# Optimization experiments

Measured on AMD Instinct MI355X. Metric: run time of the kernel, lower is better.

## Reference

```python
import jax, jax.numpy as jnp
import numpy as np

N_NODES = 50000
N_EDGES = 640000
D_IN, D_HID, D_OUT = 128, 256, 2


def setup_inputs() -> dict:
    key = jax.random.key(0)
    ks = jax.random.split(key, 8)
    node_features = jax.random.normal(ks[0], (N_NODES, D_IN), dtype=jnp.float32)
    src = jax.random.randint(ks[1], (N_EDGES,), 0, N_NODES)
    dst = jax.random.randint(ks[2], (N_EDGES,), 0, N_NODES)
    s_in = 1.0 / np.sqrt(D_IN)
    s_hid = 1.0 / np.sqrt(D_HID)
    return {
        "node_features": node_features,
        "src": src,
        "dst": dst,
        "W1_self": jax.random.normal(ks[3], (D_IN, D_HID), dtype=jnp.float32) * s_in,
        "W1_neigh": jax.random.normal(ks[4], (D_IN, D_HID), dtype=jnp.float32) * s_in,
        "b1": jnp.zeros((D_HID,), dtype=jnp.float32),
        "W2_self": jax.random.normal(ks[5], (D_HID, D_OUT), dtype=jnp.float32) * s_hid,
        "W2_neigh": jax.random.normal(ks[6], (D_HID, D_OUT), dtype=jnp.float32) * s_hid,
        "b2": jnp.zeros((D_OUT,), dtype=jnp.float32),
    }


def _sage_mean(x, src, dst, W_self, W_neigh, b, n_nodes):
    # gather source-node features along edges, mean-reduce into destinations
    msg = x[src]                                                  # [E, D]
    agg = jax.ops.segment_sum(msg, dst, num_segments=n_nodes)     # [N, D]
    deg = jax.ops.segment_sum(jnp.ones((src.shape[0], 1), x.dtype), dst,
                              num_segments=n_nodes)               # [N, 1]
    h_neigh = agg / jnp.maximum(deg, 1.0)
    return x @ W_self + h_neigh @ W_neigh + b


def reference(node_features, src, dst, W1_self, W1_neigh, b1, W2_self, W2_neigh, b2):
    h = _sage_mean(node_features, src, dst, W1_self, W1_neigh, b1, N_NODES)
    h = jax.nn.relu(h)
    logits = _sage_mean(h, src, dst, W2_self, W2_neigh, b2, N_NODES)
    return logits
```

## Files before the change

kernel.cpp:

```cpp
#include <hip/hip_runtime.h>

#define D_IN 128
#define D_HID 256
#define CH 1024
#define MPAD 50048

typedef short bf16x8 __attribute__((ext_vector_type(8)));
typedef float f32x4 __attribute__((ext_vector_type(4)));

__device__ __forceinline__ unsigned short f2bf_rne(float x) {
  unsigned int u = __float_as_uint(x);
  unsigned int r = (u + 0x7FFFu + ((u >> 16) & 1u)) >> 16;
  return (unsigned short)r;
}
__device__ __forceinline__ float bf2f(unsigned short b) {
  return __uint_as_float(((unsigned int)b) << 16);
}

__global__ void k_hist(const int* __restrict__ dst, int* __restrict__ deg, int E) {
  int e = blockIdx.x * blockDim.x + threadIdx.x;
  if (e < E) atomicAdd(&deg[dst[e]], 1);
}

__global__ __launch_bounds__(256) void k_csum(const int* __restrict__ deg,
                                              int* __restrict__ csum, int n) {
  __shared__ int ws[4];
  int t = threadIdx.x, lane = t & 63, w = t >> 6;
  int base = blockIdx.x * CH + t * 4;
  int s = 0;
  #pragma unroll
  for (int j = 0; j < 4; ++j) { int i = base + j; s += (i < n) ? deg[i] : 0; }
  #pragma unroll
  for (int off = 32; off > 0; off >>= 1) s += __shfl_down(s, off, 64);
  if (lane == 0) ws[w] = s;
  __syncthreads();
  if (t == 0) csum[blockIdx.x] = ws[0] + ws[1] + ws[2] + ws[3];
}

__global__ void k_coff(const int* __restrict__ csum, int* __restrict__ coff, int nb) {
  int lane = threadIdx.x & 63;
  int v = (lane < nb) ? csum[lane] : 0;
  int x = v;
  #pragma unroll
  for (int off = 1; off < 64; off <<= 1) {
    int u = __shfl_up(x, off, 64);
    if (lane >= off) x += u;
  }
  if (lane < nb) coff[lane] = x - v;
}

__global__ __launch_bounds__(256) void k_scanw(const int* __restrict__ deg,
                                               const int* __restrict__ coff,
                                               int* __restrict__ rs, int n) {
  __shared__ int ws[4];
  int t = threadIdx.x, lane = t & 63, w = t >> 6;
  int base = blockIdx.x * CH + t * 4;
  int d[4];
  #pragma unroll
  for (int j = 0; j < 4; ++j) { int i = base + j; d[j] = (i < n) ? deg[i] : 0; }
  int tt = d[0] + d[1] + d[2] + d[3];
  int x = tt;
  #pragma unroll
  for (int off = 1; off < 64; off <<= 1) {
    int u = __shfl_up(x, off, 64);
    if (lane >= off) x += u;
  }
  if (lane == 63) ws[w] = x;
  __syncthreads();
  if (t == 0) { int s = 0;
    #pragma unroll
    for (int j = 0; j < 4; ++j) { int tmp = ws[j]; ws[j] = s; s += tmp; } }
  __syncthreads();
  int excl = ws[w] + (x - tt) + coff[blockIdx.x];
  #pragma unroll
  for (int j = 0; j < 4; ++j) {
    int i = base + j;
    excl += d[j];
    if (i < n) rs[i + 1] = excl;
  }
  if (blockIdx.x == 0 && t == 0) rs[0] = 0;
}

__global__ void k_scatter(const int* __restrict__ src, const int* __restrict__ dst,
                          const int* __restrict__ rs, int* __restrict__ cursor,
                          int* __restrict__ esrc, int E) {
  int e = blockIdx.x * blockDim.x + threadIdx.x;
  if (e < E) {
    int d = dst[e];
    int pos = rs[d] + atomicAdd(&cursor[d], 1);
    esrc[pos] = src[e];
  }
}

__global__ __launch_bounds__(256) void k_convW(const float* __restrict__ W1s,
                                               const float* __restrict__ W1n,
                                               unsigned short* __restrict__ Bth,
                                               unsigned short* __restrict__ Btl) {
  int k = blockIdx.x;
  int col = threadIdx.x;
  float w = (k < 128) ? W1s[(size_t)k * D_HID + col]
                      : W1n[(size_t)(k - 128) * D_HID + col];
  unsigned short hi = f2bf_rne(w);
  unsigned short lo = f2bf_rne(w - bf2f(hi));
  Bth[(size_t)col * 256 + k] = hi;
  Btl[(size_t)col * 256 + k] = lo;
}

__global__ __launch_bounds__(256) void k_convX(const float* __restrict__ X,
                                               unsigned short* __restrict__ Ah,
                                               unsigned short* __restrict__ Al,
                                               int n) {
  int row = blockIdx.x * 4 + (threadIdx.x >> 6);
  int lane = threadIdx.x & 63;
  unsigned short* ah = Ah + (size_t)row * 256 + lane * 2;
  unsigned short* al = Al + (size_t)row * 256 + lane * 2;
  if (row < n) {
    float2 v = *(const float2*)(X + (size_t)row * D_IN + lane * 2);
    unsigned short hx = f2bf_rne(v.x), hy = f2bf_rne(v.y);
    unsigned short lx = f2bf_rne(v.x - bf2f(hx)), ly = f2bf_rne(v.y - bf2f(hy));
    *(ushort2*)ah = make_ushort2(hx, hy);
    *(ushort2*)al = make_ushort2(lx, ly);
  } else {
    ushort2 z = make_ushort2(0, 0);
    *(ushort2*)ah = z; *(ushort2*)(ah + 128) = z;
    *(ushort2*)al = z; *(ushort2*)(al + 128) = z;
  }
}

__global__ void k_agg1(const float* __restrict__ X, const int* __restrict__ rs,
                       const int* __restrict__ esrc,
                       unsigned short* __restrict__ Ah,
                       unsigned short* __restrict__ Al, int n) {
  int wid = (blockIdx.x * blockDim.x + threadIdx.x) >> 6;
  int lane = threadIdx.x & 63;
  if (wid >= n) return;
  int s0 = rs[wid], s1 = rs[wid + 1];
  float ax0 = 0.f, ay0 = 0.f, ax1 = 0.f, ay1 = 0.f;
  int e = s0;
  for (; e + 3 < s1; e += 4) {
    int i0 = esrc[e + 0], i1 = esrc[e + 1], i2 = esrc[e + 2], i3 = esrc[e + 3];
    float2 v0 = *(const float2*)(X + (size_t)i0 * D_IN + lane * 2);
    float2 v1 = *(const float2*)(X + (size_t)i1 * D_IN + lane * 2);
    float2 v2 = *(const float2*)(X + (size_t)i2 * D_IN + lane * 2);
    float2 v3 = *(const float2*)(X + (size_t)i3 * D_IN + lane * 2);
    ax0 += v0.x; ay0 += v0.y;
    ax1 += v1.x; ay1 += v1.y;
    ax0 += v2.x; ay0 += v2.y;
    ax1 += v3.x; ay1 += v3.y;
  }
  for (; e < s1; ++e) {
    int s = esrc[e];
    float2 v = *(const float2*)(X + (size_t)s * D_IN + lane * 2);
    ax0 += v.x; ay0 += v.y;
  }
  int d = s1 - s0;
  float inv = 1.0f / (float)(d > 1 ? d : 1);
  float mx = (ax0 + ax1) * inv, my = (ay0 + ay1) * inv;
  unsigned short hx = f2bf_rne(mx), hy = f2bf_rne(my);
  unsigned short lx = f2bf_rne(mx - bf2f(hx)), ly = f2bf_rne(my - bf2f(hy));
  *(ushort2*)(Ah + (size_t)wid * 256 + 128 + lane * 2) = make_ushort2(hx, hy);
  *(ushort2*)(Al + (size_t)wid * 256 + 128 + lane * 2) = make_ushort2(lx, ly);
}

#define AS1 __attribute__((address_space(1)))
#define AS3 __attribute__((address_space(3)))

__global__ __launch_bounds__(256, 3) void k_gemm1(
    const unsigned short* __restrict__ Ah, const unsigned short* __restrict__ Al,
    const unsigned short* __restrict__ Bth, const unsigned short* __restrict__ Btl,
    const float* __restrict__ b1, const float* __restrict__ W2s,
    const float* __restrict__ W2n, float* __restrict__ SP) {
  __shared__ unsigned short sAh[128][32];
  __shared__ unsigned short sAl[128][32];
  __shared__ unsigned short sBh[128][32];
  __shared__ unsigned short sBl[128][32];

  const int tid = threadIdx.x;
  const int w = tid >> 6;
  const int l = tid & 63;
  const int wm = w & 1, wn = w >> 1;
  const int m0 = blockIdx.x * 128;
  const int n0 = blockIdx.y * 128;

  f32x4 acc[4][4];
  #pragma unroll
  for (int i = 0; i < 4; ++i)
    #pragma unroll
    for (int j = 0; j < 4; ++j) acc[i][j] = (f32x4)0.f;

  const int rsub = l >> 2;
  const int ksub = (l & 3) * 8;
  const int g = l >> 4;
  const int c = l & 15;
  const int kb = g * 8;

  for (int kt = 0; kt < 256; kt += 32) {
    #pragma unroll
    for (int j = 0; j < 2; ++j) {
      int r = w * 32 + j * 16;
      const unsigned short* ga = Ah + (size_t)(m0 + r + rsub) * 256 + kt + ksub;
      const unsigned short* gb = Al + (size_t)(m0 + r + rsub) * 256 + kt + ksub;
      const unsigned short* gc = Bth + (size_t)(n0 + r + rsub) * 256 + kt + ksub;
      const unsigned short* gd = Btl + (size_t)(n0 + r + rsub) * 256 + kt + ksub;
      __builtin_amdgcn_global_load_lds((AS1 const void*)ga, (AS3 void*)&sAh[r][0], 16, 0, 0);
      __builtin_amdgcn_global_load_lds((AS1 const void*)gb, (AS3 void*)&sAl[r][0], 16, 0, 0);
      __builtin_amdgcn_global_load_lds((AS1 const void*)gc, (AS3 void*)&sBh[r][0], 16, 0, 0);
      __builtin_amdgcn_global_load_lds((AS1 const void*)gd, (AS3 void*)&sBl[r][0], 16, 0, 0);
    }
    __syncthreads();

    bf16x8 ahi[4], alo[4];
    #pragma unroll
    for (int mi = 0; mi < 4; ++mi) {
      int arow = wm * 64 + mi * 16 + c;
      ahi[mi] = *(const bf16x8*)(&sAh[arow][kb]);
      alo[mi] = *(const bf16x8*)(&sAl[arow][kb]);
    }
    #pragma unroll
    for (int ni = 0; ni < 4; ++ni) {
      int bcol = wn * 64 + ni * 16 + c;
      bf16x8 bhi = *(const bf16x8*)(&sBh[bcol][kb]);
      bf16x8 blo = *(const bf16x8*)(&sBl[bcol][kb]);
      #pragma unroll
      for (int mi = 0; mi < 4; ++mi) {
        acc[mi][ni] = __builtin_amdgcn_mfma_f32_16x16x32_bf16(ahi[mi], bhi, acc[mi][ni], 0, 0, 0);
        acc[mi][ni] = __builtin_amdgcn_mfma_f32_16x16x32_bf16(ahi[mi], blo, acc[mi][ni], 0, 0, 0);
        acc[mi][ni] = __builtin_amdgcn_mfma_f32_16x16x32_bf16(alo[mi], bhi, acc[mi][ni], 0, 0, 0);
      }
    }
    __syncthreads();
  }

  float b1v[4]; float2 w2sv[4], w2nv[4];
  #pragma unroll
  for (int ni = 0; ni < 4; ++ni) {
    int col = n0 + wn * 64 + ni * 16 + c;
    b1v[ni] = b1[col];
    w2sv[ni] = *(const float2*)(W2s + (size_t)col * 2);
    w2nv[ni] = *(const float2*)(W2n + (size_t)col * 2);
  }
  #pragma unroll
  for (int mi = 0; mi < 4; ++mi) {
    #pragma unroll
    for (int j = 0; j < 4; ++j) {
      float s0 = 0.f, s1 = 0.f, p0 = 0.f, p1 = 0.f;
      #pragma unroll
      for (int ni = 0; ni < 4; ++ni) {
        float h = fmaxf(acc[mi][ni][j] + b1v[ni], 0.f);
        s0 += h * w2sv[ni].x; s1 += h * w2sv[ni].y;
        p0 += h * w2nv[ni].x; p1 += h * w2nv[ni].y;
      }
      #pragma unroll
      for (int off = 1; off < 16; off <<= 1) {
        s0 += __shfl_xor(s0, off, 64);
        s1 += __shfl_xor(s1, off, 64);
        p0 += __shfl_xor(p0, off, 64);
        p1 += __shfl_xor(p1, off, 64);
      }
      if (c == 0) {
        int row = m0 + wm * 64 + mi * 16 + g * 4 + j;
        float* sp = SP + (size_t)row * 4;
        atomicAdd(sp + 0, s0);
        atomicAdd(sp + 1, s1);
        atomicAdd(sp + 2, p0);
        atomicAdd(sp + 3, p1);
      }
    }
  }
}

__global__ void k_agg2(const float* __restrict__ SP,
                       const int* __restrict__ rs, const int* __restrict__ esrc,
                       const float* __restrict__ b2,
                       float* __restrict__ out, int n) {
  int nid = blockIdx.x * blockDim.x + threadIdx.x;
  if (nid >= n) return;
  int s0 = rs[nid], s1 = rs[nid + 1];
  float a00 = 0.f, a01 = 0.f, a10 = 0.f, a11 = 0.f;
  int e = s0;
  for (; e + 3 < s1; e += 4) {
    int i0 = esrc[e + 0], i1 = esrc[e + 1], i2 = esrc[e + 2], i3 = esrc[e + 3];
    float2 p0 = *(const float2*)(SP + (size_t)i0 * 4 + 2);
    float2 p1 = *(const float2*)(SP + (size_t)i1 * 4 + 2);
    float2 p2 = *(const float2*)(SP + (size_t)i2 * 4 + 2);
    float2 p3 = *(const float2*)(SP + (size_t)i3 * 4 + 2);
    a00 += p0.x; a01 += p0.y;
    a10 += p1.x; a11 += p1.y;
    a00 += p2.x; a01 += p2.y;
    a10 += p3.x; a11 += p3.y;
  }
  for (; e < s1; ++e) {
    int s = esrc[e];
    float2 p = *(const float2*)(SP + (size_t)s * 4 + 2);
    a00 += p.x; a01 += p.y;
  }
  int d = s1 - s0;
  float inv = 1.0f / (float)(d > 1 ? d : 1);
  float2 sv = *(const float2*)(SP + (size_t)nid * 4);
  float2 o;
  o.x = sv.x + b2[0] + (a00 + a10) * inv;
  o.y = sv.y + b2[1] + (a01 + a11) * inv;
  *(float2*)(out + (size_t)nid * 2) = o;
}

extern "C" void kernel_launch(void* const* d_in, const int* in_sizes, int n_in,
                              void* d_out, int out_size, void* d_ws, size_t ws_size,
                              hipStream_t stream) {
  const float* X   = (const float*)d_in[0];
  const int*   src = (const int*)d_in[1];
  const int*   dst = (const int*)d_in[2];
  const float* W1s = (const float*)d_in[3];
  const float* W1n = (const float*)d_in[4];
  const float* b1  = (const float*)d_in[5];
  const float* W2s = (const float*)d_in[6];
  const float* W2n = (const float*)d_in[7];
  const float* b2  = (const float*)d_in[8];
  float* out = (float*)d_out;

  const int N = in_sizes[0] / D_IN;
  const int E = in_sizes[1];
  const int NB = (N + CH - 1) / CH;

  int* deg    = (int*)d_ws;
  int* cursor = deg + N;
  int* rs     = cursor + N;
  int* csum   = rs + (N + 8);
  int* coff   = csum + 64;
  int* esrc   = coff + 64;
  float* SP   = (float*)(esrc + E);
  unsigned short* Ah  = (unsigned short*)(SP + (size_t)MPAD * 4);
  unsigned short* Al  = Ah + (size_t)MPAD * 256;
  unsigned short* Bth = Al + (size_t)MPAD * 256;
  unsigned short* Btl = Bth + 256 * 256;

  hipMemsetAsync(deg, 0, sizeof(int) * (size_t)2 * N, stream);
  hipMemsetAsync(SP, 0, sizeof(float) * (size_t)MPAD * 4, stream);

  int eb = (E + 255) / 256;
  k_convW  <<<256, 256, 0, stream>>>(W1s, W1n, Bth, Btl);
  k_convX  <<<MPAD / 4, 256, 0, stream>>>(X, Ah, Al, N);
  k_hist   <<<eb, 256, 0, stream>>>(dst, deg, E);
  k_csum   <<<NB, 256, 0, stream>>>(deg, csum, N);
  k_coff   <<<1, 64, 0, stream>>>(csum, coff, NB);
  k_scanw  <<<NB, 256, 0, stream>>>(deg, coff, rs, N);
  k_scatter<<<eb, 256, 0, stream>>>(src, dst, rs, cursor, esrc, E);
  k_agg1   <<<(N + 3) / 4, 256, 0, stream>>>(X, rs, esrc, Ah, Al, N);
  k_gemm1  <<<dim3(MPAD / 128, 2), 256, 0, stream>>>(Ah, Al, Bth, Btl,
                                                     b1, W2s, W2n, SP);
  k_agg2   <<<(N + 255) / 256, 256, 0, stream>>>(SP, rs, esrc, b2, out, N);
}
```

Baseline: 303.4 us.

## Fuse X bf16 split into GEMM, retile to full-width N, drop atomics

Removes the separate k_convX pass: the GEMM reads fp32 X directly, splits it into hi/lo bf16 in registers and writes it to LDS, while the aggregated half comes from a compact 128-wide Mh/Ml buffer. The GEMM is retiled so each block covers 64 rows and all 256 output columns, with each wave owning 16 rows. Because every row's partial layer-2 products are then complete within one block, SP is written with plain float4 stores instead of atomics, and the SP memset is dropped. The trade-off is a smaller M tile with less B reuse per block, and the K loop is not software-pipelined, so each step waits on its loads.

```diff
diff --git a/kernel.cpp b/kernel.cpp
--- a/kernel.cpp
+++ b/kernel.cpp
@@ -7,6 +7,10 @@
 
 typedef short bf16x8 __attribute__((ext_vector_type(8)));
 typedef float f32x4 __attribute__((ext_vector_type(4)));
+typedef unsigned short ushort8 __attribute__((ext_vector_type(8)));
+
+#define AS1 __attribute__((address_space(1)))
+#define AS3 __attribute__((address_space(3)))
 
 __device__ __forceinline__ unsigned short f2bf_rne(float x) {
   unsigned int u = __float_as_uint(x);
@@ -106,31 +110,10 @@
   Btl[(size_t)col * 256 + k] = lo;
 }
 
-__global__ __launch_bounds__(256) void k_convX(const float* __restrict__ X,
-                                               unsigned short* __restrict__ Ah,
-                                               unsigned short* __restrict__ Al,
-                                               int n) {
-  int row = blockIdx.x * 4 + (threadIdx.x >> 6);
-  int lane = threadIdx.x & 63;
-  unsigned short* ah = Ah + (size_t)row * 256 + lane * 2;
-  unsigned short* al = Al + (size_t)row * 256 + lane * 2;
-  if (row < n) {
-    float2 v = *(const float2*)(X + (size_t)row * D_IN + lane * 2);
-    unsigned short hx = f2bf_rne(v.x), hy = f2bf_rne(v.y);
-    unsigned short lx = f2bf_rne(v.x - bf2f(hx)), ly = f2bf_rne(v.y - bf2f(hy));
-    *(ushort2*)ah = make_ushort2(hx, hy);
-    *(ushort2*)al = make_ushort2(lx, ly);
-  } else {
-    ushort2 z = make_ushort2(0, 0);
-    *(ushort2*)ah = z; *(ushort2*)(ah + 128) = z;
-    *(ushort2*)al = z; *(ushort2*)(al + 128) = z;
-  }
-}
-
 __global__ void k_agg1(const float* __restrict__ X, const int* __restrict__ rs,
                        const int* __restrict__ esrc,
-                       unsigned short* __restrict__ Ah,
-                       unsigned short* __restrict__ Al, int n) {
+                       unsigned short* __restrict__ Mh,
+                       unsigned short* __restrict__ Ml, int n) {
   int wid = (blockIdx.x * blockDim.x + threadIdx.x) >> 6;
   int lane = threadIdx.x & 63;
   if (wid >= n) return;
@@ -158,113 +141,111 @@
   float mx = (ax0 + ax1) * inv, my = (ay0 + ay1) * inv;
   unsigned short hx = f2bf_rne(mx), hy = f2bf_rne(my);
   unsigned short lx = f2bf_rne(mx - bf2f(hx)), ly = f2bf_rne(my - bf2f(hy));
-  *(ushort2*)(Ah + (size_t)wid * 256 + 128 + lane * 2) = make_ushort2(hx, hy);
-  *(ushort2*)(Al + (size_t)wid * 256 + 128 + lane * 2) = make_ushort2(lx, ly);
-}
-
-#define AS1 __attribute__((address_space(1)))
-#define AS3 __attribute__((address_space(3)))
+  *(ushort2*)(Mh + (size_t)wid * 128 + lane * 2) = make_ushort2(hx, hy);
+  *(ushort2*)(Ml + (size_t)wid * 128 + lane * 2) = make_ushort2(lx, ly);
+}
 
 __global__ __launch_bounds__(256, 3) void k_gemm1(
-    const unsigned short* __restrict__ Ah, const unsigned short* __restrict__ Al,
+    const float* __restrict__ X,
+    const unsigned short* __restrict__ Mh, const unsigned short* __restrict__ Ml,
     const unsigned short* __restrict__ Bth, const unsigned short* __restrict__ Btl,
     const float* __restrict__ b1, const float* __restrict__ W2s,
-    const float* __restrict__ W2n, float* __restrict__ SP) {
-  __shared__ unsigned short sAh[128][32];
-  __shared__ unsigned short sAl[128][32];
-  __shared__ unsigned short sBh[128][32];
-  __shared__ unsigned short sBl[128][32];
+    const float* __restrict__ W2n, float* __restrict__ SP, int n) {
+  __shared__ __align__(16) unsigned short sAh[4][512];
+  __shared__ __align__(16) unsigned short sAl[4][512];
+  __shared__ __align__(16) unsigned short sBh[16][512];
+  __shared__ __align__(16) unsigned short sBl[16][512];
 
   const int tid = threadIdx.x;
   const int w = tid >> 6;
   const int l = tid & 63;
-  const int wm = w & 1, wn = w >> 1;
-  const int m0 = blockIdx.x * 128;
-  const int n0 = blockIdx.y * 128;
-
-  f32x4 acc[4][4];
-  #pragma unroll
-  for (int i = 0; i < 4; ++i)
-    #pragma unroll
-    for (int j = 0; j < 4; ++j) acc[i][j] = (f32x4)0.f;
-
-  const int rsub = l >> 2;
-  const int ksub = (l & 3) * 8;
+  const int c = l & 15;
   const int g = l >> 4;
-  const int c = l & 15;
-  const int kb = g * 8;
-
-  for (int kt = 0; kt < 256; kt += 32) {
-    #pragma unroll
-    for (int j = 0; j < 2; ++j) {
-      int r = w * 32 + j * 16;
-      const unsigned short* ga = Ah + (size_t)(m0 + r + rsub) * 256 + kt + ksub;
-      const unsigned short* gb = Al + (size_t)(m0 + r + rsub) * 256 + kt + ksub;
-      const unsigned short* gc = Bth + (size_t)(n0 + r + rsub) * 256 + kt + ksub;
-      const unsigned short* gd = Btl + (size_t)(n0 + r + rsub) * 256 + kt + ksub;
-      __builtin_amdgcn_global_load_lds((AS1 const void*)ga, (AS3 void*)&sAh[r][0], 16, 0, 0);
-      __builtin_amdgcn_global_load_lds((AS1 const void*)gb, (AS3 void*)&sAl[r][0], 16, 0, 0);
-      __builtin_amdgcn_global_load_lds((AS1 const void*)gc, (AS3 void*)&sBh[r][0], 16, 0, 0);
-      __builtin_amdgcn_global_load_lds((AS1 const void*)gd, (AS3 void*)&sBl[r][0], 16, 0, 0);
+  const int m0 = blockIdx.x * 64;
+
+  f32x4 acc[16];
+  #pragma unroll
+  for (int i = 0; i < 16; ++i) acc[i] = (f32x4)0.f;
+
+  const int arow = m0 + w * 16 + c;
+  const int xrow = (arow < n) ? arow : (n - 1);
+
+  for (int ks = 0; ks < 8; ++ks) {
+    const int kt = ks * 32;
+    if (kt < 128) {
+      const float* src = X + (size_t)xrow * D_IN + kt + g * 8;
+      float4 u0 = *(const float4*)(src);
+      float4 u1 = *(const float4*)(src + 4);
+      float v[8] = {u0.x, u0.y, u0.z, u0.w, u1.x, u1.y, u1.z, u1.w};
+      ushort8 hh, ll;
+      #pragma unroll
+      for (int i = 0; i < 8; ++i) {
+        unsigned short h = f2bf_rne(v[i]);
+        hh[i] = h;
+        ll[i] = f2bf_rne(v[i] - bf2f(h));
+      }
+      *(ushort8*)(&sAh[w][l * 8]) = hh;
+      *(ushort8*)(&sAl[w][l * 8]) = ll;
+    } else {
+      const unsigned short* mh = Mh + (size_t)arow * 128 + (kt - 128) + g * 8;
+      const unsigned short* ml = Ml + (size_t)arow * 128 + (kt - 128) + g * 8;
+      __builtin_amdgcn_global_load_lds((AS1 const void*)mh, (AS3 void*)&sAh[w][0], 16, 0, 0);
+      __builtin_amdgcn_global_load_lds((AS1 const void*)ml, (AS3 void*)&sAl[w][0], 16, 0, 0);
+    }
+    #pragma unroll
+    for (int q = 0; q < 4; ++q) {
+      int ni = w * 4 + q;
+      const unsigned short* bh = Bth + (size_t)(ni * 16 + c) * 256 + kt + g * 8;
+      const unsigned short* bl = Btl + (size_t)(ni * 16 + c) * 256 + kt + g * 8;
+      __builtin_amdgcn_global_load_lds((AS1 const void*)bh, (AS3 void*)&sBh[ni][0], 16, 0, 0);
+      __builtin_amdgcn_global_load_lds((AS1 const void*)bl, (AS3 void*)&sBl[ni][0], 16, 0, 0);
     }
     __syncthreads();
 
-    bf16x8 ahi[4], alo[4];
-    #pragma unroll
-    for (int mi = 0; mi < 4; ++mi) {
-      int arow = wm * 64 + mi * 16 + c;
-      ahi[mi] = *(const bf16x8*)(&sAh[arow][kb]);
-      alo[mi] = *(const bf16x8*)(&sAl[arow][kb]);
-    }
-    #pragma unroll
-    for (int ni = 0; ni < 4; ++ni) {
-      int bcol = wn * 64 + ni * 16 + c;
-      bf16x8 bhi = *(const bf16x8*)(&sBh[bcol][kb]);
-      bf16x8 blo = *(const bf16x8*)(&sBl[bcol][kb]);
-      #pragma unroll
-      for (int mi = 0; mi < 4; ++mi) {
-        acc[mi][ni] = __builtin_amdgcn_mfma_f32_16x16x32_bf16(ahi[mi], bhi, acc[mi][ni], 0, 0, 0);
-        acc[mi][ni] = __builtin_amdgcn_mfma_f32_16x16x32_bf16(ahi[mi], blo, acc[mi][ni], 0, 0, 0);
-        acc[mi][ni] = __builtin_amdgcn_mfma_f32_16x16x32_bf16(alo[mi], bhi, acc[mi][ni], 0, 0, 0);
-      }
+    bf16x8 ah = *(const bf16x8*)(&sAh[w][l * 8]);
+    bf16x8 al = *(const bf16x8*)(&sAl[w][l * 8]);
+    #pragma unroll
+    for (int ni = 0; ni < 16; ++ni) {
+      bf16x8 bh = *(const bf16x8*)(&sBh[ni][l * 8]);
+      bf16x8 bl = *(const bf16x8*)(&sBl[ni][l * 8]);
+      acc[ni] = __builtin_amdgcn_mfma_f32_16x16x32_bf16(ah, bh, acc[ni], 0, 0, 0);
+      acc[ni] = __builtin_amdgcn_mfma_f32_16x16x32_bf16(ah, bl, acc[ni], 0, 0, 0);
+      acc[ni] = __builtin_amdgcn_mfma_f32_16x16x32_bf16(al, bh, acc[ni], 0, 0, 0);
     }
     __syncthreads();
   }
 
-  float b1v[4]; float2 w2sv[4], w2nv[4];
-  #pragma unroll
-  for (int ni = 0; ni < 4; ++ni) {
-    int col = n0 + wn * 64 + ni * 16 + c;
-    b1v[ni] = b1[col];
-    w2sv[ni] = *(const float2*)(W2s + (size_t)col * 2);
-    w2nv[ni] = *(const float2*)(W2n + (size_t)col * 2);
-  }
-  #pragma unroll
-  for (int mi = 0; mi < 4; ++mi) {
+  float s0[4] = {0.f, 0.f, 0.f, 0.f}, s1[4] = {0.f, 0.f, 0.f, 0.f};
+  float p0[4] = {0.f, 0.f, 0.f, 0.f}, p1[4] = {0.f, 0.f, 0.f, 0.f};
+  #pragma unroll
+  for (int ni = 0; ni < 16; ++ni) {
+    int col = ni * 16 + c;
+    float bb = b1[col];
+    float2 ws = *(const float2*)(W2s + (size_t)col * 2);
+    float2 wn = *(const float2*)(W2n + (size_t)col * 2);
     #pragma unroll
     for (int j = 0; j < 4; ++j) {
-      float s0 = 0.f, s1 = 0.f, p0 = 0.f, p1 = 0.f;
-      #pragma unroll
-      for (int ni = 0; ni < 4; ++ni) {
-        float h = fmaxf(acc[mi][ni][j] + b1v[ni], 0.f);
-        s0 += h * w2sv[ni].x; s1 += h * w2sv[ni].y;
-        p0 += h * w2nv[ni].x; p1 += h * w2nv[ni].y;
-      }
-      #pragma unroll
-      for (int off = 1; off < 16; off <<= 1) {
-        s0 += __shfl_xor(s0, off, 64);
-        s1 += __shfl_xor(s1, off, 64);
-        p0 += __shfl_xor(p0, off, 64);
-        p1 += __shfl_xor(p1, off, 64);
-      }
-      if (c == 0) {
-        int row = m0 + wm * 64 + mi * 16 + g * 4 + j;
-        float* sp = SP + (size_t)row * 4;
-        atomicAdd(sp + 0, s0);
-        atomicAdd(sp + 1, s1);
-        atomicAdd(sp + 2, p0);
-        atomicAdd(sp + 3, p1);
-      }
+      float h = fmaxf(acc[ni][j] + bb, 0.f);
+      s0[j] += h * ws.x; s1[j] += h * ws.y;
+      p0[j] += h * wn.x; p1[j] += h * wn.y;
+    }
+  }
+  #pragma unroll
+  for (int j = 0; j < 4; ++j) {
+    #pragma unroll
+    for (int off = 1; off < 16; off <<= 1) {
+      s0[j] += __shfl_xor(s0[j], off, 64);
+      s1[j] += __shfl_xor(s1[j], off, 64);
+      p0[j] += __shfl_xor(p0[j], off, 64);
+      p1[j] += __shfl_xor(p1[j], off, 64);
+    }
+  }
+  if (c == 0) {
+    #pragma unroll
+    for (int j = 0; j < 4; ++j) {
+      int row = m0 + w * 16 + g * 4 + j;
+      float4 o; o.x = s0[j]; o.y = s1[j]; o.z = p0[j]; o.w = p1[j];
+      *(float4*)(SP + (size_t)row * 4) = o;
     }
   }
 }
@@ -328,24 +309,22 @@
   int* coff   = csum + 64;
   int* esrc   = coff + 64;
   float* SP   = (float*)(esrc + E);
-  unsigned short* Ah  = (unsigned short*)(SP + (size_t)MPAD * 4);
-  unsigned short* Al  = Ah + (size_t)MPAD * 256;
-  unsigned short* Bth = Al + (size_t)MPAD * 256;
+  unsigned short* Mh  = (unsigned short*)(SP + (size_t)MPAD * 4);
+  unsigned short* Ml  = Mh + (size_t)MPAD * 128;
+  unsigned short* Bth = Ml + (size_t)MPAD * 128;
   unsigned short* Btl = Bth + 256 * 256;
 
   hipMemsetAsync(deg, 0, sizeof(int) * (size_t)2 * N, stream);
-  hipMemsetAsync(SP, 0, sizeof(float) * (size_t)MPAD * 4, stream);
 
   int eb = (E + 255) / 256;
   k_convW  <<<256, 256, 0, stream>>>(W1s, W1n, Bth, Btl);
-  k_convX  <<<MPAD / 4, 256, 0, stream>>>(X, Ah, Al, N);
   k_hist   <<<eb, 256, 0, stream>>>(dst, deg, E);
   k_csum   <<<NB, 256, 0, stream>>>(deg, csum, N);
   k_coff   <<<1, 64, 0, stream>>>(csum, coff, NB);
   k_scanw  <<<NB, 256, 0, stream>>>(deg, coff, rs, N);
   k_scatter<<<eb, 256, 0, stream>>>(src, dst, rs, cursor, esrc, E);
-  k_agg1   <<<(N + 3) / 4, 256, 0, stream>>>(X, rs, esrc, Ah, Al, N);
-  k_gemm1  <<<dim3(MPAD / 128, 2), 256, 0, stream>>>(Ah, Al, Bth, Btl,
-                                                     b1, W2s, W2n, SP);
+  k_agg1   <<<(N + 3) / 4, 256, 0, stream>>>(X, rs, esrc, Mh, Ml, N);
+  k_gemm1  <<<MPAD / 64, 256, 0, stream>>>(X, Mh, Ml, Bth, Btl,
+                                           b1, W2s, W2n, SP, N);
   k_agg2   <<<(N + 255) / 256, 256, 0, stream>>>(SP, rs, esrc, b2, out, N);
 }
```

New measurement: 255.4 us. 1.19x faster.
